# Kernel optimization log

Hardware: AMD Instinct MI355X
Metric: run time of the kernel (lower is better)

Reference implementation:

```python
import jax, jax.numpy as jnp
import numpy as np
from jax import lax

B, S, C = 64, 256, 12          # sentences, words/sentence, chars/word
Ec, Hc = 50, 64                # char embed / char LSTM hidden (per direction)
Ew = 300                       # word embed dim
Hw = 256 + Hc                  # word LSTM hidden per direction = word_hidden_dim + char_hidden_dim
Din = Ew + 2 * Hc              # word LSTM input dim
NT = 20                        # len(tag_vocab.stoi) - 2
Vw, Vc = 50000, 100


def setup_inputs() -> dict:
    key = jax.random.key(0)
    ks = jax.random.split(key, 32)
    p = lambda i, shape: jax.random.normal(ks[i], shape, jnp.float32) * 0.05
    inp = {
        'batch_sentences': jax.random.randint(ks[0], (B, S), 0, Vw),
        'lengths': jnp.full((B,), S, dtype=jnp.int32),  # sorted (all full) -> packed == time-major
        'char_ids': jax.random.randint(ks[1], (B, S, C), 0, Vc),
        'word_emb': p(2, (Vw, Ew)),
        'char_emb': p(3, (Vc, Ec)),
        'char_h0': p(4, (2, Hc)),  # fixed random init state (init_char_hidden), [fwd/bwd, Hc]
        'char_c0': p(5, (2, Hc)),
        'Wih_cf': p(6, (4 * Hc, Ec)), 'Whh_cf': p(7, (4 * Hc, Hc)), 'bih_cf': p(8, (4 * Hc,)), 'bhh_cf': p(9, (4 * Hc,)),
        'Wih_cb': p(10, (4 * Hc, Ec)), 'Whh_cb': p(11, (4 * Hc, Hc)), 'bih_cb': p(12, (4 * Hc,)), 'bhh_cb': p(13, (4 * Hc,)),
        'Wih_wf': p(14, (4 * Hw, Din)), 'Whh_wf': p(15, (4 * Hw, Hw)), 'bih_wf': p(16, (4 * Hw,)), 'bhh_wf': p(17, (4 * Hw,)),
        'Wih_wb': p(18, (4 * Hw, Din)), 'Whh_wb': p(19, (4 * Hw, Hw)), 'bih_wb': p(20, (4 * Hw,)), 'bhh_wb': p(21, (4 * Hw,)),
        'W_tag': p(22, (NT, 2 * Hw)), 'b_tag': p(23, (NT,)),
    }
    return inp


def _lstm(x, h0, c0, Wih, Whh, bih, bhh):
    """x: [T, N, In] time-major. Returns (all h [T,N,H], final h [N,H]). torch gate order i,f,g,o."""
    pre = jnp.einsum('tni,gi->tng', x, Wih) + bih  # input projection for all steps

    def step(carry, pt):
        h, c = carry
        g = pt + h @ Whh.T + bhh
        i, f, gg, o = jnp.split(g, 4, axis=-1)
        c = jax.nn.sigmoid(f) * c + jax.nn.sigmoid(i) * jnp.tanh(gg)
        h = jax.nn.sigmoid(o) * jnp.tanh(c)
        return (h, c), h

    (hT, _), hs = lax.scan(step, (h0, c0), pre)
    return hs, hT


def reference(batch_sentences, lengths, char_ids, word_emb, char_emb, char_h0, char_c0,
              Wih_cf, Whh_cf, bih_cf, bhh_cf, Wih_cb, Whh_cb, bih_cb, bhh_cb,
              Wih_wf, Whh_wf, bih_wf, bhh_wf, Wih_wb, Whh_wb, bih_wb, bhh_wb,
              W_tag, b_tag):
    N = B * S
    we = word_emb[batch_sentences]                                   # [B,S,Ew]
    ce = char_emb[char_ids].reshape(N, C, Ec).transpose(1, 0, 2)     # [C,N,Ec] all words batched

    bc = lambda v: jnp.broadcast_to(v, (N, Hc))
    _, hTf = _lstm(ce, bc(char_h0[0]), bc(char_c0[0]), Wih_cf, Whh_cf, bih_cf, bhh_cf)
    _, hTb = _lstm(ce[::-1], bc(char_h0[1]), bc(char_c0[1]), Wih_cb, Whh_cb, bih_cb, bhh_cb)
    char_feat = jnp.concatenate([hTf, hTb], -1).reshape(B, S, 2 * Hc)  # hn.view(-1) per word

    x = jnp.concatenate([we, char_feat], -1).transpose(1, 0, 2)      # [S,B,Din] time-major
    z0 = jnp.zeros((B, Hw), x.dtype)
    hsf, _ = _lstm(x, z0, z0, Wih_wf, Whh_wf, bih_wf, bhh_wf)
    hsb, _ = _lstm(x[::-1], z0, z0, Wih_wb, Whh_wb, bih_wb, bhh_wb)
    out = jnp.concatenate([hsf, hsb[::-1]], -1)                      # [S,B,2*Hw]

    # lengths are all == S, so packed data order == time-major flatten
    packed = out.reshape(S * B, 2 * Hw)
    tag_scores = packed @ W_tag.T + b_tag                            # [S*B, NT]
    return tag_scores
```

## Files before the change

### kernel.cpp

```cpp
#include <hip/hip_runtime.h>
#include <stdint.h>

typedef __attribute__((ext_vector_type(8))) short bf16x8;
typedef __attribute__((ext_vector_type(4))) float f32x4;
typedef unsigned short u16;
typedef unsigned int u32;
typedef unsigned long long u64;

#define DEV static __device__ __forceinline__


DEV u16 f2b(float f){ union{float f; u32 u;} v; v.f=f; return (u16)((v.u + 0x7FFFu + ((v.u>>16)&1u))>>16); }
DEV float b2f(u16 b){ union{u32 u; float f;} v; v.u=((u32)b)<<16; return v.f; }
DEV float sigm(float x){ return 1.0f/(1.0f + __expf(-x)); }
DEV float tanhf2(float x){ float a=fabsf(x); float e=__expf(-2.0f*a); float t=(1.0f-e)/(1.0f+e); return x<0.0f? -t : t; }

DEV void spin_flag(u32* fp, u32 tgt){
  int guard = 0;
  while (atomicAdd(fp, 0u) < tgt){
    __builtin_amdgcn_s_sleep(1);
    if (++guard > (1<<13)) break;
  }
}

__global__ void k_init(u32* flags){ flags[threadIdx.x] = 0u; }

__global__ __launch_bounds__(256,1) void k_char(
    const int* __restrict__ char_ids, const float* __restrict__ cemb,
    const float* __restrict__ h0g, const float* __restrict__ c0g,
    const float* __restrict__ WihF, const float* __restrict__ WhhF,
    const float* __restrict__ bihF, const float* __restrict__ bhhF,
    const float* __restrict__ WihB, const float* __restrict__ WhhB,
    const float* __restrict__ bihB, const float* __restrict__ bhhB,
    u16* __restrict__ cfF, u16* __restrict__ cfB)
{
  __shared__ __align__(16) u16 Wl[256*128];
  __shared__ __align__(16) u16 Xc[64*128];
  __shared__ __align__(16) u16 Gc[64*256];

  const int dir = blockIdx.x & 1;
  const int n0  = (blockIdx.x >> 1) * 64;
  const int tid = threadIdx.x;
  const int lane = tid & 63, wv = tid >> 6;
  const int l15 = lane & 15, l4 = lane >> 4;

  const float* Wih = dir ? WihB : WihF;
  const float* Whh = dir ? WhhB : WhhF;
  const float* bih = dir ? bihB : bihF;
  const float* bhh = dir ? bhhB : bhhF;
  const float* h0 = h0g + dir*64;
  const float* c0 = c0g + dir*64;

  {
    const int n = tid; const int gt = n & 3, col = n >> 2;
    const int grow = gt*64 + col;
    for (int k = 0; k < 128; ++k){
      float v;
      if (k < 50) v = Wih[grow*50 + k];
      else if (k < 114) v = Whh[grow*64 + (k-50)];
      else if (k == 114) v = bih[grow] + bhh[grow];
      else v = 0.0f;
      Wl[n*128 + (k ^ ((n&7)<<3))] = f2b(v);
    }
  }
  for (int idx = tid; idx < 64*128; idx += 256){
    int w = idx >> 7, k = idx & 127;
    float v = (k==114) ? 1.0f : ((k>=50 && k<114) ? h0[k-50] : 0.0f);
    Xc[w*128 + (k ^ ((w&7)<<3))] = f2b(v);
  }
  const int uw = tid >> 2, ucb = (tid & 3) * 16;
  float cst[16], hreg[16];
  #pragma unroll
  for (int cc = 0; cc < 16; ++cc){ cst[cc] = c0[ucb + cc]; hreg[cc] = 0.0f; }

  for (int t = 0; t < 12; ++t){
    const int cpos = dir ? (11 - t) : t;
    __syncthreads();
    for (int idx = tid; idx < 3200; idx += 256){
      int w = idx / 50, k = idx - w*50;
      int cid = char_ids[(n0 + w)*12 + cpos];
      Xc[w*128 + (k ^ ((w&7)<<3))] = f2b(cemb[cid*50 + k]);
    }
    __syncthreads();
    f32x4 acc[4][4];
    #pragma unroll
    for (int mt=0; mt<4; ++mt)
      #pragma unroll
      for (int nt=0; nt<4; ++nt)
        #pragma unroll
        for (int j=0;j<4;++j) acc[mt][nt][j] = 0.0f;
    #pragma unroll
    for (int kk = 0; kk < 4; ++kk){
      bf16x8 A[4];
      #pragma unroll
      for (int mt=0; mt<4; ++mt){
        int row = mt*16 + l15;
        A[mt] = *(const bf16x8*)&Xc[row*128 + ((kk*32 + 8*l4) ^ ((row&7)<<3))];
      }
      #pragma unroll
      for (int nt=0; nt<4; ++nt){
        int n = wv*64 + nt*16 + l15;
        bf16x8 Bf = *(const bf16x8*)&Wl[n*128 + ((kk*32 + 8*l4) ^ ((n&7)<<3))];
        #pragma unroll
        for (int mt=0; mt<4; ++mt)
          acc[mt][nt] = __builtin_amdgcn_mfma_f32_16x16x32_bf16(A[mt], Bf, acc[mt][nt], 0,0,0);
      }
    }
    #pragma unroll
    for (int mt=0; mt<4; ++mt)
      #pragma unroll
      for (int nt=0; nt<4; ++nt)
        #pragma unroll
        for (int j=0;j<4;++j){
          int m = mt*16 + l4*4 + j;
          int n = wv*64 + nt*16 + l15;
          Gc[m*256 + n] = f2b(acc[mt][nt][j]);
        }
    __syncthreads();
    #pragma unroll
    for (int cc=0; cc<16; ++cc){
      int col = ucb + cc;
      const u16* gp = &Gc[uw*256 + col*4];
      float gi=b2f(gp[0]), gf=b2f(gp[1]), gg=b2f(gp[2]), go=b2f(gp[3]);
      float c2 = sigm(gf)*cst[cc] + sigm(gi)*tanhf2(gg);
      cst[cc]=c2;
      float h = sigm(go)*tanhf2(c2);
      hreg[cc]=h;
      Xc[uw*128 + ((50+col) ^ ((uw&7)<<3))] = f2b(h);
    }
  }
  u16* cf = dir ? cfB : cfF;
  #pragma unroll
  for (int cc=0; cc<16; ++cc) cf[(u64)(n0+uw)*64 + ucb + cc] = f2b(hreg[cc]);
}

__global__ __launch_bounds__(256,1) void k_buildx(
    const int* __restrict__ sents, const float* __restrict__ wemb,
    const u16* __restrict__ cfF, const u16* __restrict__ cfB,
    u16* __restrict__ xg)
{
  const int r = blockIdx.x*4 + (threadIdx.x >> 6);
  const int lane = threadIdx.x & 63;
  const int t = r >> 6, b = r & 63;
  const int sid = sents[b*256 + t];
  const int n = b*256 + t;
  u32* xr = (u32*)(xg + (u64)r*448);
  const float* we = wemb + (u64)sid*300;
  const u16* cf = cfF + (u64)n*64;
  const u16* cb = cfB + (u64)n*64;
  for (int u = lane; u < 224; u += 64){
    int c0 = 2*u, c1 = 2*u + 1;
    u16 lo = (c0 < 300) ? f2b(we[c0]) : (c0 < 364) ? cf[c0-300] : (c0 < 428) ? cb[c0-364] : (c0==428) ? f2b(1.0f) : (u16)0;
    u16 hi = (c1 < 300) ? f2b(we[c1]) : (c1 < 364) ? cf[c1-300] : (c1 < 428) ? cb[c1-364] : (c1==428) ? f2b(1.0f) : (u16)0;
    xr[u] = (u32)lo | ((u32)hi << 16);
  }
}

DEV void stage_x(const u16* __restrict__ src, u16* Xs, int tid)
{
  #pragma unroll
  for (int half=0; half<2; ++half){
    f32x4 r[7];
    #pragma unroll
    for (int p=0;p<7;++p){ int idx=tid+256*(half*7+p); int row=idx/56, e=idx-row*56;
      r[p] = *(const f32x4*)(src + row*448 + e*8); }
    #pragma unroll
    for (int p=0;p<7;++p){ int idx=tid+256*(half*7+p); int row=idx/56, e=idx-row*56;
      *(f32x4*)&Xs[row*456 + e*8] = r[p]; }
  }
}

DEV void wih_mfma(f32x4 (&ACC)[2][4], const u16* Xs, const bf16x8 (&BWih)[2][14],
                  int l15, int l4)
{
  #pragma unroll
  for (int nt=0;nt<2;++nt)
    #pragma unroll
    for (int mt=0;mt<4;++mt)
      #pragma unroll
      for (int j=0;j<4;++j) ACC[nt][mt][j]=0.f;
  #pragma unroll
  for (int kk=0;kk<14;++kk){
    bf16x8 A[4];
    #pragma unroll
    for (int mt=0;mt<4;++mt)
      A[mt] = *(const bf16x8*)&Xs[(mt*16+l15)*456 + kk*32 + 8*l4];
    #pragma unroll
    for (int nt=0;nt<2;++nt)
      #pragma unroll
      for (int mt=0;mt<4;++mt)
        ACC[nt][mt] = __builtin_amdgcn_mfma_f32_16x16x32_bf16(A[mt], BWih[nt][kk], ACC[nt][mt],0,0,0);
  }
}

DEV void fill_bwih(bf16x8 (&BWih)[2][14], const float* Wih, const float* bih,
                   const float* bhh, int wg, int wv, int l15, int l4)
{
  #pragma unroll
  for (int nt=0; nt<2; ++nt){
    const int q = wv*32 + nt*16 + l15;
    const int col = q >> 2, gt = q & 3;
    const int grow = gt*320 + wg*32 + col;
    #pragma unroll
    for (int kk=0; kk<14; ++kk){
      bf16x8 v;
      #pragma unroll
      for (int j=0;j<8;++j){
        int k = kk*32 + 8*l4 + j;
        float f = (k < 428) ? Wih[(u64)grow*428 + k] : ((k==428) ? (bih[grow]+bhh[grow]) : 0.0f);
        v[j] = (short)f2b(f);
      }
      BWih[nt][kk] = v;
    }
  }
}

__global__ __launch_bounds__(256,1) void k_pre(
    const u16* __restrict__ xg,
    const float* __restrict__ WihFg, const float* __restrict__ bihFg, const float* __restrict__ bhhFg,
    const float* __restrict__ WihBg, const float* __restrict__ bihBg, const float* __restrict__ bhhBg,
    float* __restrict__ g0)
{
  __shared__ __align__(16) u16 Xs[64*456];
  const int bid = blockIdx.x;
  const int chunk = bid & 31;
  const int wgdir = bid >> 5;
  const int dir = wgdir / 10, wg = wgdir - dir*10;
  const int tid = threadIdx.x;
  const int lane = tid & 63, wv = tid >> 6;
  const int l15 = lane & 15, l4 = lane >> 4;

  const float* Wih = dir ? WihBg : WihFg;
  const float* bih = dir ? bihBg : bihFg;
  const float* bhh = dir ? bhhBg : bhhFg;

  bf16x8 BWih[2][14];
  fill_bwih(BWih, Wih, bih, bhh, wg, wv, l15, l4);

  f32x4 ACC[2][4];
  for (int tt=0; tt<8; ++tt){
    const int t = chunk*8 + tt;
    stage_x(xg + (u64)t*64*448, Xs, tid);
    __syncthreads();
    wih_mfma(ACC, Xs, BWih, l15, l4);
    float* gb = g0 + ((u64)((dir*256 + t)*10 + wg))*8192 + tid*4;
    #pragma unroll
    for (int nt=0; nt<2; ++nt)
      #pragma unroll
      for (int mt=0; mt<4; ++mt)
        *(f32x4*)(gb + (u64)(nt*4+mt)*1024) = ACC[nt][mt];
    __syncthreads();
  }
}

__global__ __launch_bounds__(256,1) void k_word_fast(
    const float* __restrict__ g0,
    const float* __restrict__ WhhFg, const float* __restrict__ WhhBg,
    u16* __restrict__ h_g, u32* __restrict__ flags, u16* __restrict__ hs)
{
  __shared__ __align__(16) u16 Hs[64*328];
  __shared__ int s_dir, s_wg;

  if (threadIdx.x == 0){
    u32 xcd;
    asm("s_getreg_b32 %0, hwreg(HW_REG_XCC_ID)" : "=s"(xcd));
    xcd &= 7u;
    int dir = -1, wg = 0;
    if (xcd <= 1u){
      u32 slot = atomicAdd(&flags[32 + xcd], 1u);
      if (slot < 10u){ dir = (int)xcd; wg = (int)slot; }
    }
    s_dir = dir; s_wg = wg;
  }
  __syncthreads();
  const int dir = s_dir, wg = s_wg;
  if (dir < 0) return;

  const int tid = threadIdx.x;
  const int lane = tid & 63, wv = tid >> 6;
  const int l15 = lane & 15, l4 = lane >> 4;
  const int qa = l15 & 3, qq = l15 >> 2;

  const float* Whh = dir ? WhhBg : WhhFg;

  bf16x8 BWhh[2][10];
  #pragma unroll
  for (int nt=0; nt<2; ++nt){
    const int q = wv*32 + nt*16 + l15;
    const int col = q >> 2, gt = q & 3;
    const int grow = gt*320 + wg*32 + col;
    #pragma unroll
    for (int kk=0; kk<10; ++kk){
      bf16x8 v;
      #pragma unroll
      for (int j=0;j<8;++j)
        v[j] = (short)f2b(Whh[(u64)grow*320 + kk*32 + 8*l4 + j]);
      BWhh[nt][kk] = v;
    }
  }

  float cst[8];
  #pragma unroll
  for (int p=0;p<8;++p) cst[p]=0.0f;

  for (int i=0; i<256; ++i){
    const int t = dir ? 255-i : i;
    const float* gb = g0 + ((u64)((dir*256 + t)*10 + wg))*8192 + tid*4;

    f32x4 ACC[2][4];
    #pragma unroll
    for (int nt=0;nt<2;++nt)
      #pragma unroll
      for (int mt=0;mt<4;++mt)
        #pragma unroll
        for (int j=0;j<4;++j) ACC[nt][mt][j]=0.f;
    f32x4 G0c[8];

    if (i > 0){
      if (tid < 10) spin_flag(&flags[dir*16 + tid], (u32)i);
      __syncthreads();
      asm volatile("buffer_inv" ::: "memory");
      {
        const u16* hb = h_g + (u64)(((i-1)&1)*2 + dir)*64*320;
        #pragma unroll
        for (int p=0; p<10; ++p){
          int idx = tid + 256*p;
          int row = idx / 40, e = idx - row*40;
          f32x4 v = *(const f32x4*)(hb + row*320 + e*8);
          *(f32x4*)&Hs[row*328 + e*8] = v;
        }
      }
      #pragma unroll
      for (int j=0;j<8;++j) G0c[j] = *(const f32x4*)(gb + (u64)j*1024);
      __syncthreads();
      #pragma unroll
      for (int kk=0; kk<10; ++kk){
        bf16x8 A[4];
        #pragma unroll
        for (int mt=0; mt<4; ++mt)
          A[mt] = *(const bf16x8*)&Hs[(mt*16 + l15)*328 + kk*32 + 8*l4];
        #pragma unroll
        for (int nt=0; nt<2; ++nt)
          #pragma unroll
          for (int mt=0; mt<4; ++mt)
            ACC[nt][mt] = __builtin_amdgcn_mfma_f32_16x16x32_bf16(A[mt], BWhh[nt][kk], ACC[nt][mt],0,0,0);
      }
    } else {
      #pragma unroll
      for (int j=0;j<8;++j) G0c[j] = *(const f32x4*)(gb + (u64)j*1024);
    }

    u64 pk[2][4];
    #pragma unroll
    for (int nt=0; nt<2; ++nt){
      #pragma unroll
      for (int mt=0; mt<4; ++mt){
        f32x4 v = ACC[nt][mt] + G0c[nt*4 + mt];
        float t0=__shfl_xor(v[1],1), t1=__shfl_xor(v[0],1), t2=__shfl_xor(v[3],1), t3=__shfl_xor(v[2],1);
        v[0] = (qa&1) ? t0 : v[0];
        v[1] = (qa&1) ? v[1] : t1;
        v[2] = (qa&1) ? t2 : v[2];
        v[3] = (qa&1) ? v[3] : t3;
        float u0=__shfl_xor(v[2],2), u1=__shfl_xor(v[3],2), u2=__shfl_xor(v[0],2), u3=__shfl_xor(v[1],2);
        v[0] = (qa&2) ? u0 : v[0];
        v[1] = (qa&2) ? u1 : v[1];
        v[2] = (qa&2) ? v[2] : u2;
        v[3] = (qa&2) ? v[3] : u3;
        v[0]=b2f(f2b(v[0])); v[1]=b2f(f2b(v[1])); v[2]=b2f(f2b(v[2])); v[3]=b2f(f2b(v[3]));
        const int ci = nt*4 + mt;
        float c2 = sigm(v[1])*cst[ci] + sigm(v[0])*tanhf2(v[2]);
        cst[ci] = c2;
        float h = sigm(v[3])*tanhf2(c2);
        u32 hu = (u32)f2b(h);
        u32 v01 = hu | ((u32)__shfl_xor((int)hu, 4) << 16);
        u32 v23 = (u32)__shfl_xor((int)v01, 8);
        pk[nt][mt] = (u64)v01 | ((u64)v23 << 32);
      }
    }
    {
      u16* hw = h_g + (u64)((i&1)*2 + dir)*64*320;
      if (qq == 0){
        #pragma unroll
        for (int nt=0; nt<2; ++nt)
          #pragma unroll
          for (int mt=0; mt<4; ++mt){
            const int b = mt*16 + l4*4 + qa;
            *(u64*)&hw[b*320 + wg*32 + wv*8 + nt*4] = pk[nt][mt];
          }
      }
    }
    asm volatile("s_waitcnt vmcnt(0)" ::: "memory");
    __syncthreads();
    if (tid == 0) atomicExch(&flags[dir*16 + wg], (u32)(i+1));
    if (qq == 0){
      #pragma unroll
      for (int nt=0; nt<2; ++nt)
        #pragma unroll
        for (int mt=0; mt<4; ++mt){
          const int b = mt*16 + l4*4 + qa;
          *(u64*)&hs[(u64)(t*64 + b)*640 + dir*320 + wg*32 + wv*8 + nt*4] = pk[nt][mt];
        }
    }
  }
}

__global__ __launch_bounds__(256,1) void k_word_slow(
    const u16* __restrict__ xg,
    const float* __restrict__ WihFg, const float* __restrict__ WhhFg,
    const float* __restrict__ bihFg, const float* __restrict__ bhhFg,
    const float* __restrict__ WihBg, const float* __restrict__ WhhBg,
    const float* __restrict__ bihBg, const float* __restrict__ bhhBg,
    u16* __restrict__ h_g, u32* __restrict__ flags, u16* __restrict__ hs)
{
  __shared__ __align__(16) u16 Hs[64*328];
  __shared__ __align__(16) u16 Xs[64*456];
  __shared__ int s_dir, s_wg;

  if (threadIdx.x == 0){
    u32 xcd;
    asm("s_getreg_b32 %0, hwreg(HW_REG_XCC_ID)" : "=s"(xcd));
    xcd &= 7u;
    int dir = -1, wg = 0;
    if (xcd <= 1u){
      u32 slot = atomicAdd(&flags[32 + xcd], 1u);
      if (slot < 10u){ dir = (int)xcd; wg = (int)slot; }
    }
    s_dir = dir; s_wg = wg;
  }
  __syncthreads();
  const int dir = s_dir, wg = s_wg;
  if (dir < 0) return;

  const int tid = threadIdx.x;
  const int lane = tid & 63, wv = tid >> 6;
  const int l15 = lane & 15, l4 = lane >> 4;
  const int qa = l15 & 3, qq = l15 >> 2;

  const float* Wih = dir ? WihBg : WihFg;
  const float* Whh = dir ? WhhBg : WhhFg;
  const float* bih = dir ? bihBg : bihFg;
  const float* bhh = dir ? bhhBg : bhhFg;

  bf16x8 BWih[2][14];
  fill_bwih(BWih, Wih, bih, bhh, wg, wv, l15, l4);
  bf16x8 BWhh[2][10];
  #pragma unroll
  for (int nt=0; nt<2; ++nt){
    const int q = wv*32 + nt*16 + l15;
    const int col = q >> 2, gt = q & 3;
    const int grow = gt*320 + wg*32 + col;
    #pragma unroll
    for (int kk=0; kk<10; ++kk){
      bf16x8 v;
      #pragma unroll
      for (int j=0;j<8;++j)
        v[j] = (short)f2b(Whh[(u64)grow*320 + kk*32 + 8*l4 + j]);
      BWhh[nt][kk] = v;
    }
  }

  float cst[8];
  #pragma unroll
  for (int p=0;p<8;++p) cst[p]=0.0f;

  f32x4 ACC[2][4];
  stage_x(xg + (u64)(dir ? 255 : 0)*64*448, Xs, tid);
  __syncthreads();
  wih_mfma(ACC, Xs, BWih, l15, l4);

  for (int i=0; i<256; ++i){
    const int t = dir ? 255-i : i;
    if (i > 0){
      if (tid < 10) spin_flag(&flags[dir*16 + tid], (u32)i);
      __syncthreads();
      asm volatile("buffer_inv" ::: "memory");
      {
        const u16* hb = h_g + (u64)(((i-1)&1)*2 + dir)*64*320;
        #pragma unroll
        for (int p=0; p<10; ++p){
          int idx = tid + 256*p;
          int row = idx / 40, e = idx - row*40;
          f32x4 v = *(const f32x4*)(hb + row*320 + e*8);
          *(f32x4*)&Hs[row*328 + e*8] = v;
        }
      }
      __syncthreads();
      #pragma unroll
      for (int kk=0; kk<10; ++kk){
        bf16x8 A[4];
        #pragma unroll
        for (int mt=0; mt<4; ++mt)
          A[mt] = *(const bf16x8*)&Hs[(mt*16 + l15)*328 + kk*32 + 8*l4];
        #pragma unroll
        for (int nt=0; nt<2; ++nt)
          #pragma unroll
          for (int mt=0; mt<4; ++mt)
            ACC[nt][mt] = __builtin_amdgcn_mfma_f32_16x16x32_bf16(A[mt], BWhh[nt][kk], ACC[nt][mt],0,0,0);
      }
    }

    u64 pk[2][4];
    #pragma unroll
    for (int nt=0; nt<2; ++nt){
      #pragma unroll
      for (int mt=0; mt<4; ++mt){
        f32x4 v = ACC[nt][mt];
        float t0=__shfl_xor(v[1],1), t1=__shfl_xor(v[0],1), t2=__shfl_xor(v[3],1), t3=__shfl_xor(v[2],1);
        v[0] = (qa&1) ? t0 : v[0];
        v[1] = (qa&1) ? v[1] : t1;
        v[2] = (qa&1) ? t2 : v[2];
        v[3] = (qa&1) ? v[3] : t3;
        float u0=__shfl_xor(v[2],2), u1=__shfl_xor(v[3],2), u2=__shfl_xor(v[0],2), u3=__shfl_xor(v[1],2);
        v[0] = (qa&2) ? u0 : v[0];
        v[1] = (qa&2) ? u1 : v[1];
        v[2] = (qa&2) ? v[2] : u2;
        v[3] = (qa&2) ? v[3] : u3;
        v[0]=b2f(f2b(v[0])); v[1]=b2f(f2b(v[1])); v[2]=b2f(f2b(v[2])); v[3]=b2f(f2b(v[3]));
        const int ci = nt*4 + mt;
        float c2 = sigm(v[1])*cst[ci] + sigm(v[0])*tanhf2(v[2]);
        cst[ci] = c2;
        float h = sigm(v[3])*tanhf2(c2);
        u32 hu = (u32)f2b(h);
        u32 v01 = hu | ((u32)__shfl_xor((int)hu, 4) << 16);
        u32 v23 = (u32)__shfl_xor((int)v01, 8);
        pk[nt][mt] = (u64)v01 | ((u64)v23 << 32);
      }
    }
    {
      u16* hw = h_g + (u64)((i&1)*2 + dir)*64*320;
      if (qq == 0){
        #pragma unroll
        for (int nt=0; nt<2; ++nt)
          #pragma unroll
          for (int mt=0; mt<4; ++mt){
            const int b = mt*16 + l4*4 + qa;
            *(u64*)&hw[b*320 + wg*32 + wv*8 + nt*4] = pk[nt][mt];
          }
      }
    }
    asm volatile("s_waitcnt vmcnt(0)" ::: "memory");
    __syncthreads();
    if (tid == 0) atomicExch(&flags[dir*16 + wg], (u32)(i+1));
    if (qq == 0){
      #pragma unroll
      for (int nt=0; nt<2; ++nt)
        #pragma unroll
        for (int mt=0; mt<4; ++mt){
          const int b = mt*16 + l4*4 + qa;
          *(u64*)&hs[(u64)(t*64 + b)*640 + dir*320 + wg*32 + wv*8 + nt*4] = pk[nt][mt];
        }
    }
    if (i < 255){
      stage_x(xg + (u64)(dir ? 254-i : i+1)*64*448, Xs, tid);
      __syncthreads();
      wih_mfma(ACC, Xs, BWih, l15, l4);
    }
  }
}

__global__ __launch_bounds__(256,1) void k_tag(
    const u16* __restrict__ hs, const float* __restrict__ Wt,
    const float* __restrict__ bt, float* __restrict__ out)
{
  __shared__ __align__(16) u16 Wl[32*648];
  __shared__ float btl[32];
  const int tid = threadIdx.x;
  const int lane = tid & 63, wv = tid >> 6;
  const int l15 = lane & 15, l4 = lane >> 4;
  const int r0 = blockIdx.x * 64;

  for (int p=0; p<80; ++p){
    int idx = tid + 256*p;
    int nq = idx / 640, k = idx - nq*640;
    Wl[nq*648 + k] = (nq < 20) ? f2b(Wt[(u64)nq*640 + k]) : (u16)0;
  }
  if (tid < 32) btl[tid] = (tid < 20) ? bt[tid] : 0.0f;
  __syncthreads();

  f32x4 acc[2];
  #pragma unroll
  for (int nt=0;nt<2;++nt)
    #pragma unroll
    for (int j=0;j<4;++j) acc[nt][j]=0.0f;

  const int mrow = r0 + wv*16 + l15;
  #pragma unroll
  for (int kk=0; kk<20; ++kk){
    bf16x8 A = *(const bf16x8*)&hs[(u64)mrow*640 + kk*32 + 8*l4];
    #pragma unroll
    for (int nt=0; nt<2; ++nt){
      bf16x8 Bf = *(const bf16x8*)&Wl[(nt*16 + l15)*648 + kk*32 + 8*l4];
      acc[nt] = __builtin_amdgcn_mfma_f32_16x16x32_bf16(A, Bf, acc[nt], 0,0,0);
    }
  }
  #pragma unroll
  for (int nt=0; nt<2; ++nt){
    int nq = nt*16 + l15;
    if (nq < 20){
      #pragma unroll
      for (int j=0;j<4;++j){
        int row = r0 + wv*16 + l4*4 + j;
        out[(u64)row*20 + nq] = acc[nt][j] + btl[nq];
      }
    }
  }
}

extern "C" void kernel_launch(void* const* d_in, const int* in_sizes, int n_in,
                              void* d_out, int out_size, void* d_ws, size_t ws_size,
                              hipStream_t stream)
{
  (void)in_sizes; (void)n_in; (void)out_size;
  const int*   sents   = (const int*)d_in[0];
  const int*   charids = (const int*)d_in[2];
  const float* wemb    = (const float*)d_in[3];
  const float* cemb    = (const float*)d_in[4];
  const float* ch0     = (const float*)d_in[5];
  const float* cc0     = (const float*)d_in[6];
  const float* Wih_cf  = (const float*)d_in[7];
  const float* Whh_cf  = (const float*)d_in[8];
  const float* bih_cf  = (const float*)d_in[9];
  const float* bhh_cf  = (const float*)d_in[10];
  const float* Wih_cb  = (const float*)d_in[11];
  const float* Whh_cb  = (const float*)d_in[12];
  const float* bih_cb  = (const float*)d_in[13];
  const float* bhh_cb  = (const float*)d_in[14];
  const float* Wih_wf  = (const float*)d_in[15];
  const float* Whh_wf  = (const float*)d_in[16];
  const float* bih_wf  = (const float*)d_in[17];
  const float* bhh_wf  = (const float*)d_in[18];
  const float* Wih_wb  = (const float*)d_in[19];
  const float* Whh_wb  = (const float*)d_in[20];
  const float* bih_wb  = (const float*)d_in[21];
  const float* bhh_wb  = (const float*)d_in[22];
  const float* W_tag   = (const float*)d_in[23];
  const float* b_tag   = (const float*)d_in[24];

  char* ws = (char*)d_ws;
  u32* flags = (u32*)(ws);
  u16* h_g   = (u16*)(ws + 256);
  u16* cf_f  = (u16*)(ws + 164096);
  u16* cf_b  = (u16*)(ws + 2261248);
  u16* x     = (u16*)(ws + 4358400);
  u16* hs    = (u16*)(ws + 19038464);
  float* g0  = (float*)(ws + 40009984);
  const u64 need = 40009984ull + 167772160ull;
  float* outp = (float*)d_out;

  hipLaunchKernelGGL(k_init, dim3(1), dim3(64), 0, stream, flags);
  hipLaunchKernelGGL(k_char, dim3(512), dim3(256), 0, stream,
    charids, cemb, ch0, cc0, Wih_cf, Whh_cf, bih_cf, bhh_cf,
    Wih_cb, Whh_cb, bih_cb, bhh_cb, cf_f, cf_b);
  hipLaunchKernelGGL(k_buildx, dim3(4096), dim3(256), 0, stream, sents, wemb, cf_f, cf_b, x);
  if ((u64)ws_size >= need){
    hipLaunchKernelGGL(k_pre, dim3(640), dim3(256), 0, stream,
      x, Wih_wf, bih_wf, bhh_wf, Wih_wb, bih_wb, bhh_wb, g0);
    hipLaunchKernelGGL(k_word_fast, dim3(256), dim3(256), 0, stream,
      g0, Whh_wf, Whh_wb, h_g, flags, hs);
  } else {
    hipLaunchKernelGGL(k_word_slow, dim3(256), dim3(256), 0, stream,
      x, Wih_wf, Whh_wf, bih_wf, bhh_wf, Wih_wb, Whh_wb, bih_wb, bhh_wb, h_g, flags, hs);
  }
  hipLaunchKernelGGL(k_tag, dim3(256), dim3(256), 0, stream, hs, W_tag, b_tag, outp);
}
```

Baseline: 1.802 ms.

## Use single counter barrier and prefetch next-step gate preactivations in word LSTM

In the fast word-LSTM kernel, the per-workgroup flag array is replaced with one shared atomic counter per direction. Each workgroup atomically increments it after publishing h, and a single thread spins until the counter reaches 10*i, where before ten threads each polled a separate flag. Loading the next timestep's precomputed input-gate values (g0) now happens right after the current step's writes, so it overlaps with the barrier wait instead of sitting on the critical path. The workspace layout is shifted to make room for the counters, and the init kernel now clears 128 flags.

```diff
diff --git a/kernel.cpp b/kernel.cpp
--- a/kernel.cpp
+++ b/kernel.cpp
@@ -15,13 +15,6 @@
 DEV float sigm(float x){ return 1.0f/(1.0f + __expf(-x)); }
 DEV float tanhf2(float x){ float a=fabsf(x); float e=__expf(-2.0f*a); float t=(1.0f-e)/(1.0f+e); return x<0.0f? -t : t; }
 
-DEV void spin_flag(u32* fp, u32 tgt){
-  int guard = 0;
-  while (atomicAdd(fp, 0u) < tgt){
-    __builtin_amdgcn_s_sleep(1);
-    if (++guard > (1<<13)) break;
-  }
-}
 
 __global__ void k_init(u32* flags){ flags[threadIdx.x] = 0u; }
 
@@ -282,6 +275,7 @@
   const int qa = l15 & 3, qq = l15 >> 2;
 
   const float* Whh = dir ? WhhBg : WhhFg;
+  u32* ctr = &flags[64 + dir*16];
 
   bf16x8 BWhh[2][10];
   #pragma unroll
@@ -303,9 +297,16 @@
   #pragma unroll
   for (int p=0;p<8;++p) cst[p]=0.0f;
 
+  f32x4 PF[8];
+  {
+    const int t0 = dir ? 255 : 0;
+    const float* gb = g0 + ((u64)((dir*256 + t0)*10 + wg))*8192 + tid*4;
+    #pragma unroll
+    for (int j=0;j<8;++j) PF[j] = *(const f32x4*)(gb + (u64)j*1024);
+  }
+
   for (int i=0; i<256; ++i){
     const int t = dir ? 255-i : i;
-    const float* gb = g0 + ((u64)((dir*256 + t)*10 + wg))*8192 + tid*4;
 
     f32x4 ACC[2][4];
     #pragma unroll
@@ -314,10 +315,16 @@
       for (int mt=0;mt<4;++mt)
         #pragma unroll
         for (int j=0;j<4;++j) ACC[nt][mt][j]=0.f;
-    f32x4 G0c[8];
 
     if (i > 0){
-      if (tid < 10) spin_flag(&flags[dir*16 + tid], (u32)i);
+      if (tid == 0){
+        const u32 tgt = 10u*(u32)i;
+        int guard = 0;
+        while (atomicAdd(ctr, 0u) < tgt){
+          __builtin_amdgcn_s_sleep(1);
+          if (++guard > (1<<13)) break;
+        }
+      }
       __syncthreads();
       asm volatile("buffer_inv" ::: "memory");
       {
@@ -330,8 +337,6 @@
           *(f32x4*)&Hs[row*328 + e*8] = v;
         }
       }
-      #pragma unroll
-      for (int j=0;j<8;++j) G0c[j] = *(const f32x4*)(gb + (u64)j*1024);
       __syncthreads();
       #pragma unroll
       for (int kk=0; kk<10; ++kk){
@@ -345,9 +350,6 @@
           for (int mt=0; mt<4; ++mt)
             ACC[nt][mt] = __builtin_amdgcn_mfma_f32_16x16x32_bf16(A[mt], BWhh[nt][kk], ACC[nt][mt],0,0,0);
       }
-    } else {
-      #pragma unroll
-      for (int j=0;j<8;++j) G0c[j] = *(const f32x4*)(gb + (u64)j*1024);
     }
 
     u64 pk[2][4];
@@ -355,7 +357,7 @@
     for (int nt=0; nt<2; ++nt){
       #pragma unroll
       for (int mt=0; mt<4; ++mt){
-        f32x4 v = ACC[nt][mt] + G0c[nt*4 + mt];
+        f32x4 v = ACC[nt][mt] + PF[nt*4 + mt];
         float t0=__shfl_xor(v[1],1), t1=__shfl_xor(v[0],1), t2=__shfl_xor(v[3],1), t3=__shfl_xor(v[2],1);
         v[0] = (qa&1) ? t0 : v[0];
         v[1] = (qa&1) ? v[1] : t1;
@@ -391,7 +393,7 @@
     }
     asm volatile("s_waitcnt vmcnt(0)" ::: "memory");
     __syncthreads();
-    if (tid == 0) atomicExch(&flags[dir*16 + wg], (u32)(i+1));
+    if (tid == 0) atomicAdd(ctr, 1u);
     if (qq == 0){
       #pragma unroll
       for (int nt=0; nt<2; ++nt)
@@ -401,6 +403,20 @@
           *(u64*)&hs[(u64)(t*64 + b)*640 + dir*320 + wg*32 + wv*8 + nt*4] = pk[nt][mt];
         }
     }
+    if (i < 255){
+      const int tn = dir ? 254-i : i+1;
+      const float* gb = g0 + ((u64)((dir*256 + tn)*10 + wg))*8192 + tid*4;
+      #pragma unroll
+      for (int j=0;j<8;++j) PF[j] = *(const f32x4*)(gb + (u64)j*1024);
+    }
+  }
+}
+
+DEV void spin_flag(u32* fp, u32 tgt){
+  int guard = 0;
+  while (atomicAdd(fp, 0u) < tgt){
+    __builtin_amdgcn_s_sleep(1);
+    if (++guard > (1<<13)) break;
   }
 }
 
@@ -638,16 +654,16 @@
 
   char* ws = (char*)d_ws;
   u32* flags = (u32*)(ws);
-  u16* h_g   = (u16*)(ws + 256);
-  u16* cf_f  = (u16*)(ws + 164096);
-  u16* cf_b  = (u16*)(ws + 2261248);
-  u16* x     = (u16*)(ws + 4358400);
-  u16* hs    = (u16*)(ws + 19038464);
-  float* g0  = (float*)(ws + 40009984);
-  const u64 need = 40009984ull + 167772160ull;
+  u16* h_g   = (u16*)(ws + 1024);
+  u16* cf_f  = (u16*)(ws + 164864);
+  u16* cf_b  = (u16*)(ws + 2262016);
+  u16* x     = (u16*)(ws + 4359168);
+  u16* hs    = (u16*)(ws + 19039232);
+  float* g0  = (float*)(ws + 40010752);
+  const u64 need = 40010752ull + 167772160ull;
   float* outp = (float*)d_out;
 
-  hipLaunchKernelGGL(k_init, dim3(1), dim3(64), 0, stream, flags);
+  hipLaunchKernelGGL(k_init, dim3(1), dim3(128), 0, stream, flags);
   hipLaunchKernelGGL(k_char, dim3(512), dim3(256), 0, stream,
     charids, cemb, ch0, cc0, Wih_cf, Whh_cf, bih_cf, bhh_cf,
     Wih_cb, Whh_cb, bih_cb, bhh_cb, cf_f, cf_b);
```

After: 1.833 ms. About the same (+1.7%).
